# Optimization experiments

Measured on AMD Instinct MI355X. Metric: run time of the kernel, lower is better.

The kernel has to match this reference:

```python
import jax, jax.numpy as jnp
import numpy as np
from jax import lax


def setup_inputs() -> dict:
    key = jax.random.key(0)
    k1, k2 = jax.random.split(key)
    B, T, C = 8, 4096, 256
    UNITS, WINDOW = 256, 2
    x = jax.random.normal(k1, (B, T, C), dtype=jnp.float32)
    kernel = jax.random.normal(k2, (WINDOW, C, 3 * UNITS), dtype=jnp.float32) * 0.05
    bias = jnp.zeros((3 * UNITS,), dtype=jnp.float32)
    return {"x": x, "kernel": kernel, "bias": bias}


def _qrnn_forward(x, kernel, bias):
    # Causal conv1d: left-pad time axis by (window - 1).
    window = kernel.shape[0]
    xp = jnp.pad(x, ((0, 0), (window - 1, 0), (0, 0)))
    gates = lax.conv_general_dilated(
        xp, kernel, window_strides=(1,), padding='VALID',
        dimension_numbers=('NWC', 'WIO', 'NWC')) + bias
    z, f, o = jnp.split(gates, 3, axis=-1)  # each [B, T, units]
    z = jnp.tanh(z)
    f = jax.nn.sigmoid(f)

    # fo_pool: c_t = f_t * c_{t-1} + (1 - f_t) * z_t, c_0 = 0.
    # Linear recurrence -> associative scan over time with elements (a, b):
    # compose((a1,b1),(a2,b2)) = (a1*a2, a2*b1 + b2).
    def combine(e1, e2):
        a1, b1 = e1
        a2, b2 = e2
        return a1 * a2, a2 * b1 + b2

    _, c = lax.associative_scan(combine, (f, (1.0 - f) * z), axis=1)
    h = jax.nn.sigmoid(o) * c  # output gate
    return h  # return_sequences=True -> [B, T, units]


def reference(x, kernel, bias):
    return _qrnn_forward(x, kernel, bias)
```

## Files before the change

### kernel.cpp

```cpp
#include <hip/hip_runtime.h>
#include <math.h>


#define Bq 8
#define Tq 4096
#define NCq 64
#define Lq 64

typedef __attribute__((ext_vector_type(8))) _Float16 f16x8;
typedef __attribute__((ext_vector_type(4))) float f32x4;

__device__ __forceinline__ float sigmoidf_(float x) {
    return 1.f / (1.f + __expf(-x));
}
__device__ __forceinline__ float tanh_fast(float x) {
    return 1.f - 2.f / (__expf(2.f * x) + 1.f);
}
__device__ __forceinline__ unsigned short f16b(float a) {
    _Float16 h = (_Float16)a;
    return *(unsigned short*)&h;
}
__device__ __forceinline__ void gload16(const void* g, void* l) {
    __builtin_amdgcn_global_load_lds(
        (const __attribute__((address_space(1))) void*)g,
        (__attribute__((address_space(3))) void*)l, 16, 0, 0);
}

__global__ __launch_bounds__(256) void split_x(
    const float* __restrict__ x, _Float16* __restrict__ xh)
{
    int idx = blockIdx.x * 256 + threadIdx.x;
    if (idx >= Bq * 4097 * 64) return;
    int b  = idx / (4097 * 64);
    int r  = idx % (4097 * 64);
    int tp = r / 64, c4 = (r % 64) << 2;
    size_t o = ((size_t)(b * 4097 + tp) << 8) + c4;
    _Float16 h4[4] = {(_Float16)0.f, (_Float16)0.f, (_Float16)0.f, (_Float16)0.f};
    if (tp > 0) {
        const float4 v = *(const float4*)&x[((size_t)(b * 4096 + tp - 1) << 8) + c4];
        h4[0] = (_Float16)v.x; h4[1] = (_Float16)v.y;
        h4[2] = (_Float16)v.z; h4[3] = (_Float16)v.w;
    }
    *(ushort4*)&xh[o] = *(ushort4*)h4;
}

__global__ __launch_bounds__(256) void split_k(
    const float* __restrict__ kw, _Float16* __restrict__ bh)
{
    int idx = blockIdx.x * 256 + threadIdx.x;
    if (idx >= 768 * 512) return;
    int n = idx >> 9, k = idx & 511;
    bh[((size_t)n << 9) + k] = (_Float16)kw[(size_t)k * 768 + n];
}

__global__ __launch_bounds__(256) void conv_gemm(
    const _Float16* __restrict__ xh, const _Float16* __restrict__ bth,
    const float* __restrict__ bias,
    _Float16* __restrict__ Z, _Float16* __restrict__ G, _Float16* __restrict__ SO)
{
    __shared__ __align__(16) char smem[49152];
    const int tid = threadIdx.x;
    const int l = tid & 63, w = tid >> 6;
    const int wr = w >> 1, wc = w & 1;

    const int p  = blockIdx.x + (blockIdx.y << 8);
    const int Lw = (p & 7) * 192 + (p >> 3);
    const int bm = Lw & 255;
    const int by = Lw >> 8;
    const int b  = bm >> 5;
    const int t0 = (bm & 31) << 7;
    const int n0 = by << 7;

    f32x4 acc[4][4] = {};

    const int rowT   = tid >> 2;
    const int slotSw = (tid & 3) ^ ((rowT >> 1) & 3);
    size_t gaBase = ((size_t)(b * 4097 + t0 + rowT) << 8) + (slotSw << 3);
    size_t gbBase = ((size_t)(n0 + rowT) << 9) + (slotSw << 3);
    const int ldsW = w << 9;

    int offA[4], offB[4];
    const int colB = (l >> 4) << 4;
    #pragma unroll
    for (int i = 0; i < 4; ++i) {
        int ra = wr * 64 + i * 16 + (l & 15);
        offA[i] = ((ra << 6) + colB) ^ (((ra >> 1) & 3) << 4);
        int rb = wc * 64 + i * 16 + (l & 15);
        offB[i] = ((rb << 6) + colB) ^ (((rb >> 1) & 3) << 4);
    }

    auto stage = [&](int kk) {
        const int buf = kk % 3;
        _Float16* pA = (_Float16*)(smem + buf * 16384) + ldsW;
        _Float16* pB = (_Float16*)(smem + buf * 16384 + 8192) + ldsW;
        size_t ga = gaBase + (size_t)kk * 32;
        size_t gb = gbBase + (size_t)kk * 32;
        gload16(xh  + ga,          pA);
        gload16(xh  + ga + 16384,  pA + 2048);
        gload16(bth + gb,          pB);
        gload16(bth + gb + 32768,  pB + 2048);
    };

    auto compute = [&](int kk) {
        const char* bA = (const char*)smem + (kk % 3) * 16384;
        const char* bB = bA + 8192;
        f16x8 fa[4], fb[4];
        #pragma unroll
        for (int i = 0; i < 4; ++i) {
            fa[i] = *(const f16x8*)(bA + offA[i]);
            fb[i] = *(const f16x8*)(bB + offB[i]);
        }
        __builtin_amdgcn_s_setprio(1);
        #pragma unroll
        for (int mi = 0; mi < 4; ++mi)
            #pragma unroll
            for (int ni = 0; ni < 4; ++ni)
                acc[mi][ni] = __builtin_amdgcn_mfma_f32_16x16x32_f16(
                    fa[mi], fb[ni], acc[mi][ni], 0, 0, 0);
        __builtin_amdgcn_s_setprio(0);
    };

    stage(0);
    stage(1);
#define QSTEP(k, V) \
    if ((k) + 2 < 16) stage((k) + 2); \
    asm volatile("s_waitcnt vmcnt(" #V ")" ::: "memory"); \
    __builtin_amdgcn_s_barrier(); \
    compute(k); \
    asm volatile("s_waitcnt lgkmcnt(0)" ::: "memory"); \
    __builtin_amdgcn_sched_barrier(0); \
    __builtin_amdgcn_s_barrier();
    QSTEP(0, 8)  QSTEP(1, 8)  QSTEP(2, 8)  QSTEP(3, 8)
    QSTEP(4, 8)  QSTEP(5, 8)  QSTEP(6, 8)  QSTEP(7, 8)
    QSTEP(8, 8)  QSTEP(9, 8)  QSTEP(10, 8) QSTEP(11, 8)
    QSTEP(12, 8) QSTEP(13, 8) QSTEP(14, 4) QSTEP(15, 0)
#undef QSTEP

    const int gsel = by >> 1;
    float bb[4];
    #pragma unroll
    for (int ni = 0; ni < 4; ++ni)
        bb[ni] = bias[n0 + wc * 64 + ni * 16 + (l & 15)];

    unsigned short* Hd = (unsigned short*)smem;
    #pragma unroll
    for (int ni = 0; ni < 4; ++ni) {
        const int cl = wc * 64 + ni * 16 + (l & 15);
        #pragma unroll
        for (int mi = 0; mi < 4; ++mi)
            #pragma unroll
            for (int r = 0; r < 4; ++r) {
                const int trl = wr * 64 + mi * 16 + ((l >> 4) << 2) + r;
                float g = acc[mi][ni][r] + bb[ni];
                float a = (gsel == 0) ? tanh_fast(g)
                        : (gsel == 1) ? sigmoidf_(-g)
                                      : sigmoidf_(g);
                int byt = (trl << 8) + ((cl << 1) ^ (((trl >> 2) & 3) << 4));
                *(unsigned short*)((char*)Hd + byt) = f16b(a);
            }
    }
    __syncthreads();
    _Float16* Gg = (gsel == 0) ? Z : (gsel == 1) ? G : SO;
    const int u0 = n0 & 255;
    const size_t gbase = ((size_t)(b * 4096 + t0) << 8) + u0;
    #pragma unroll
    for (int j = 0; j < 8; ++j) {
        int hoff = tid * 8 + j * 2048;
        int row  = hoff >> 7;
        int cby  = (hoff & 127) << 1;
        int srcB = (row << 8) + (cby ^ (((row >> 2) & 3) << 4));
        int4 v = *(const int4*)((const char*)Hd + srcB);
        *(int4*)&Gg[gbase + ((size_t)row << 8) + (cby >> 1)] = v;
    }
}

__global__ __launch_bounds__(256) void chunk_reduce(
    const _Float16* __restrict__ Z, const _Float16* __restrict__ G,
    float* __restrict__ CA, float* __restrict__ CB)
{
    const int u = threadIdx.x;
    const int blk = blockIdx.x;
    const int b = blk >> 6, ck = blk & 63;
    size_t base = (((size_t)b << 12) + ck * Lq) * 256 + u;
    float A = 1.f, Bv = 0.f;
    #pragma unroll 8
    for (int s = 0; s < Lq; ++s) {
        size_t idx = base + (size_t)s * 256;
        float g = (float)G[idx];
        float z = (float)Z[idx];
        Bv = fmaf(1.f - g, Bv, g * z);
        A *= (1.f - g);
    }
    size_t cidx = ((size_t)b * NCq + ck) * 256 + u;
    CA[cidx] = A;
    CB[cidx] = Bv;
}

__global__ __launch_bounds__(256) void carry_scan(
    const float* __restrict__ CA, const float* __restrict__ CB,
    float* __restrict__ CIN)
{
    const int u = threadIdx.x;
    const int b = blockIdx.x;
    float c = 0.f;
    #pragma unroll 8
    for (int k = 0; k < NCq; ++k) {
        size_t idx = ((size_t)b * NCq + k) * 256 + u;
        CIN[idx] = c;
        c = fmaf(CA[idx], c, CB[idx]);
    }
}

__global__ __launch_bounds__(256) void apply_scan(
    const _Float16* __restrict__ Z, const _Float16* __restrict__ G,
    const _Float16* __restrict__ SO, const float* __restrict__ CIN,
    float* __restrict__ out)
{
    const int u = threadIdx.x;
    const int blk = blockIdx.x;
    const int b = blk >> 6, ck = blk & 63;
    float c = CIN[((size_t)b * NCq + ck) * 256 + u];
    size_t base = (((size_t)b << 12) + ck * Lq) * 256 + u;
    #pragma unroll 8
    for (int s = 0; s < Lq; ++s) {
        size_t idx = base + (size_t)s * 256;
        float g = (float)G[idx], z = (float)Z[idx];
        c = fmaf(1.f - g, c, g * z);
        out[idx] = (float)SO[idx] * c;
    }
}

extern "C" void kernel_launch(void* const* d_in, const int* in_sizes, int n_in,
                              void* d_out, int out_size, void* d_ws, size_t ws_size,
                              hipStream_t stream) {
    const float* x    = (const float*)d_in[0];
    const float* kw   = (const float*)d_in[1];
    const float* bias = (const float*)d_in[2];
    float* out = (float*)d_out;

    char* p = (char*)d_ws;
    _Float16* xh  = (_Float16*)p; p += (size_t)Bq * 4097 * 256 * 2;
    _Float16* bth = (_Float16*)p; p += (size_t)768 * 512 * 2;
    _Float16* Z   = (_Float16*)p; p += (size_t)Bq * Tq * 256 * 2;
    _Float16* G   = (_Float16*)p; p += (size_t)Bq * Tq * 256 * 2;
    _Float16* SO  = (_Float16*)p; p += (size_t)Bq * Tq * 256 * 2;
    float* CA  = (float*)p; p += (size_t)Bq * NCq * 256 * 4;
    float* CB  = (float*)p; p += (size_t)Bq * NCq * 256 * 4;
    float* CIN = (float*)p;

    split_x<<<(Bq * 4097 * 64 + 255) / 256, 256, 0, stream>>>(x, xh);
    split_k<<<(768 * 512 + 255) / 256, 256, 0, stream>>>(kw, bth);
    dim3 g1(256, 6);
    conv_gemm<<<g1, 256, 0, stream>>>(xh, bth, bias, Z, G, SO);
    chunk_reduce<<<512, 256, 0, stream>>>(Z, G, CA, CB);
    carry_scan<<<Bq, 256, 0, stream>>>(CA, CB, CIN);
    apply_scan<<<512, 256, 0, stream>>>(Z, G, SO, CIN, out);
}
```

Baseline: 87.03 us.

## Widen GEMM K-tile to 64 with double buffering and halve scan chunk length

The conv GEMM now loads 64-wide K slices into a double-buffered 64 KB LDS layout with an 8-way XOR swizzle. This halves the number of barrier-separated steps and drops the XCD-aware block remapping. Separately, the recurrence is split into 128 chunks of 32 timesteps instead of 64 of 64, doubling block count for the reduce and apply kernels. The cost is a longer serial carry scan and possible loss of L2 locality from the removed block remap.

```diff
diff --git a/kernel.cpp b/kernel.cpp
--- a/kernel.cpp
+++ b/kernel.cpp
@@ -4,8 +4,8 @@
 
 #define Bq 8
 #define Tq 4096
-#define NCq 64
-#define Lq 64
+#define NCq 128
+#define Lq 32
 
 typedef __attribute__((ext_vector_type(8))) _Float16 f16x8;
 typedef __attribute__((ext_vector_type(4))) float f32x4;
@@ -58,82 +58,81 @@
     const float* __restrict__ bias,
     _Float16* __restrict__ Z, _Float16* __restrict__ G, _Float16* __restrict__ SO)
 {
-    __shared__ __align__(16) char smem[49152];
+    __shared__ __align__(16) char smem[65536];
     const int tid = threadIdx.x;
     const int l = tid & 63, w = tid >> 6;
     const int wr = w >> 1, wc = w & 1;
-
-    const int p  = blockIdx.x + (blockIdx.y << 8);
-    const int Lw = (p & 7) * 192 + (p >> 3);
-    const int bm = Lw & 255;
-    const int by = Lw >> 8;
+    const int bm = blockIdx.x;
+    const int by = blockIdx.y;
     const int b  = bm >> 5;
     const int t0 = (bm & 31) << 7;
     const int n0 = by << 7;
 
     f32x4 acc[4][4] = {};
 
-    const int rowT   = tid >> 2;
-    const int slotSw = (tid & 3) ^ ((rowT >> 1) & 3);
-    size_t gaBase = ((size_t)(b * 4097 + t0 + rowT) << 8) + (slotSw << 3);
-    size_t gbBase = ((size_t)(n0 + rowT) << 9) + (slotSw << 3);
-    const int ldsW = w << 9;
-
-    int offA[4], offB[4];
-    const int colB = (l >> 4) << 4;
+    const int slotSw = (tid & 7) ^ ((tid >> 3) & 7);
+    size_t gaBase = ((size_t)(b * 4097 + t0 + (tid >> 3)) << 8) + slotSw * 8;
+    size_t gbBase = ((size_t)(n0 + (tid >> 3)) << 9) + slotSw * 8;
+    const int ldsD = w << 10;
+
+    int offA[4][2], offB[4][2];
     #pragma unroll
     for (int i = 0; i < 4; ++i) {
         int ra = wr * 64 + i * 16 + (l & 15);
-        offA[i] = ((ra << 6) + colB) ^ (((ra >> 1) & 3) << 4);
         int rb = wc * 64 + i * 16 + (l & 15);
-        offB[i] = ((rb << 6) + colB) ^ (((rb >> 1) & 3) << 4);
-    }
-
-    auto stage = [&](int kk) {
-        const int buf = kk % 3;
-        _Float16* pA = (_Float16*)(smem + buf * 16384) + ldsW;
-        _Float16* pB = (_Float16*)(smem + buf * 16384 + 8192) + ldsW;
-        size_t ga = gaBase + (size_t)kk * 32;
-        size_t gb = gbBase + (size_t)kk * 32;
-        gload16(xh  + ga,          pA);
-        gload16(xh  + ga + 16384,  pA + 2048);
-        gload16(bth + gb,          pB);
-        gload16(bth + gb + 32768,  pB + 2048);
+        #pragma unroll
+        for (int h = 0; h < 2; ++h) {
+            offA[i][h] = (ra << 7) + (((h * 4 + (l >> 4)) ^ (ra & 7)) << 4);
+            offB[i][h] = (rb << 7) + (((h * 4 + (l >> 4)) ^ (ra & 7)) << 4);
+        }
+    }
+
+    auto stage = [&](int buf, int kk) {
+        char* bA = smem + buf * 32768;
+        char* bB = bA + 16384;
+        const size_t kAoff = (kk < 4) ? (size_t)(kk * 64)
+                                      : (size_t)(256 + (kk - 4) * 64);
+        const size_t kBoff = (size_t)kk * 64;
+        #pragma unroll
+        for (int i = 0; i < 4; ++i) {
+            gload16(xh  + gaBase + kAoff + (size_t)i * 8192,  bA + i * 4096 + ldsD);
+            gload16(bth + gbBase + kBoff + (size_t)i * 16384, bB + i * 4096 + ldsD);
+        }
     };
 
-    auto compute = [&](int kk) {
-        const char* bA = (const char*)smem + (kk % 3) * 16384;
-        const char* bB = bA + 8192;
-        f16x8 fa[4], fb[4];
-        #pragma unroll
-        for (int i = 0; i < 4; ++i) {
-            fa[i] = *(const f16x8*)(bA + offA[i]);
-            fb[i] = *(const f16x8*)(bB + offB[i]);
+    auto compute = [&](int buf) {
+        const char* bA = smem + buf * 32768;
+        const char* bB = bA + 16384;
+        __builtin_amdgcn_s_setprio(1);
+        #pragma unroll
+        for (int h = 0; h < 2; ++h) {
+            f16x8 fa[4], fb[4];
+            #pragma unroll
+            for (int i = 0; i < 4; ++i) {
+                fa[i] = *(const f16x8*)(bA + offA[i][h]);
+                fb[i] = *(const f16x8*)(bB + offB[i][h]);
+            }
+            #pragma unroll
+            for (int mi = 0; mi < 4; ++mi)
+                #pragma unroll
+                for (int ni = 0; ni < 4; ++ni)
+                    acc[mi][ni] = __builtin_amdgcn_mfma_f32_16x16x32_f16(
+                        fa[mi], fb[ni], acc[mi][ni], 0, 0, 0);
         }
-        __builtin_amdgcn_s_setprio(1);
-        #pragma unroll
-        for (int mi = 0; mi < 4; ++mi)
-            #pragma unroll
-            for (int ni = 0; ni < 4; ++ni)
-                acc[mi][ni] = __builtin_amdgcn_mfma_f32_16x16x32_f16(
-                    fa[mi], fb[ni], acc[mi][ni], 0, 0, 0);
         __builtin_amdgcn_s_setprio(0);
     };
 
-    stage(0);
-    stage(1);
+    stage(0, 0);
 #define QSTEP(k, V) \
-    if ((k) + 2 < 16) stage((k) + 2); \
+    if ((k) < 7) stage(((k) + 1) & 1, (k) + 1); \
     asm volatile("s_waitcnt vmcnt(" #V ")" ::: "memory"); \
     __builtin_amdgcn_s_barrier(); \
-    compute(k); \
+    compute((k) & 1); \
     asm volatile("s_waitcnt lgkmcnt(0)" ::: "memory"); \
     __builtin_amdgcn_sched_barrier(0); \
     __builtin_amdgcn_s_barrier();
-    QSTEP(0, 8)  QSTEP(1, 8)  QSTEP(2, 8)  QSTEP(3, 8)
-    QSTEP(4, 8)  QSTEP(5, 8)  QSTEP(6, 8)  QSTEP(7, 8)
-    QSTEP(8, 8)  QSTEP(9, 8)  QSTEP(10, 8) QSTEP(11, 8)
-    QSTEP(12, 8) QSTEP(13, 8) QSTEP(14, 4) QSTEP(15, 0)
+    QSTEP(0, 8) QSTEP(1, 8) QSTEP(2, 8) QSTEP(3, 8)
+    QSTEP(4, 8) QSTEP(5, 8) QSTEP(6, 8) QSTEP(7, 0)
 #undef QSTEP
 
     const int gsel = by >> 1;
@@ -180,7 +179,7 @@
 {
     const int u = threadIdx.x;
     const int blk = blockIdx.x;
-    const int b = blk >> 6, ck = blk & 63;
+    const int b = blk >> 7, ck = blk & 127;
     size_t base = (((size_t)b << 12) + ck * Lq) * 256 + u;
     float A = 1.f, Bv = 0.f;
     #pragma unroll 8
@@ -218,7 +217,7 @@
 {
     const int u = threadIdx.x;
     const int blk = blockIdx.x;
-    const int b = blk >> 6, ck = blk & 63;
+    const int b = blk >> 7, ck = blk & 127;
     float c = CIN[((size_t)b * NCq + ck) * 256 + u];
     size_t base = (((size_t)b << 12) + ck * Lq) * 256 + u;
     #pragma unroll 8
@@ -252,7 +251,7 @@
     split_k<<<(768 * 512 + 255) / 256, 256, 0, stream>>>(kw, bth);
     dim3 g1(256, 6);
     conv_gemm<<<g1, 256, 0, stream>>>(xh, bth, bias, Z, G, SO);
-    chunk_reduce<<<512, 256, 0, stream>>>(Z, G, CA, CB);
+    chunk_reduce<<<1024, 256, 0, stream>>>(Z, G, CA, CB);
     carry_scan<<<Bq, 256, 0, stream>>>(CA, CB, CIN);
-    apply_scan<<<512, 256, 0, stream>>>(Z, G, SO, CIN, out);
-}
+    apply_scan<<<1024, 256, 0, stream>>>(Z, G, SO, CIN, out);
+}
```

Measured after the change: 99.13 us. +13.9%, slower.
